# Optimization experiments

Hardware: AMD Instinct MI355X
Metric: run time of the kernel (lower is better)

## Reference

```python
import jax, jax.numpy as jnp
import numpy as np

POLY_DEGREE = 2
LEVELS = 3


def setup_inputs() -> dict:
    key = jax.random.key(0)
    B, T, C = 32, 4096, 128
    x = jax.random.normal(key, (B, T, C), dtype=jnp.float32)
    return {"x": x}


def reference(x):
    B, T, C = x.shape
    t = jnp.linspace(0.0, 1.0, T, dtype=x.dtype)[:, None]          # [T,1]
    Tmat = jnp.concatenate([t ** i for i in range(POLY_DEGREE + 1)], axis=1)  # [T,d+1]
    # Least-squares solution is identical across batch & channel since the
    # design matrix is shared: sol = pinv(Tmat) @ x  (closed-form, one solve).
    P = jnp.linalg.pinv(Tmat)                                       # [d+1,T]
    coef = jnp.einsum('dt,btc->bdc', P, x)                          # [B,d+1,C]
    low = jnp.einsum('td,bdc->btc', Tmat, coef)                     # [B,T,C] trend
    res = x - low                                                   # residual
    highs = [res] + [jnp.zeros_like(res) for _ in range(LEVELS - 1)]
    return (low, highs)
```

## Files before the change

kernel.cpp:

```cpp
#include <hip/hip_runtime.h>
#include <hip/hip_cooperative_groups.h>

namespace cg = cooperative_groups;

typedef float f4 __attribute__((ext_vector_type(4)));

#define TT 4096
#define CC 128
#define BB 32
#define C4 (CC / 4)
#define NB 1024
#define ROWS_B 128
#define RECS 32

__global__ __launch_bounds__(256, 4) void k_fused(const f4* __restrict__ x4,
                                                  f4* __restrict__ partial,
                                                  f4* __restrict__ out,
                                                  float scale, float c20,
                                                  float invS0, float invS2,
                                                  float invD) {
    const size_t N4 = (size_t)BB * TT * C4;
    const int blk = blockIdx.x;
    const int b = blk >> 5;
    const int tile = blk & 31;
    const int tid = threadIdx.x;
    const int r = tid >> 5;
    const int q = tid & 31;

    __shared__ f4 red[3][8][32];
    __shared__ f4 ca[3][32];

    const size_t base = (size_t)b * TT * C4;
    const int t0 = tile * ROWS_B;
    const f4 z = (f4)0.0f;

    f4 m0 = (f4)0.0f, m1 = (f4)0.0f, m2 = (f4)0.0f;
#pragma unroll
    for (int k = 0; k < ROWS_B / 8; ++k) {
        const int t = t0 + r + (k << 3);
        const float u = fmaf((float)t, scale, -0.5f);
        const size_t idx = base + (size_t)t * C4 + q;
        const f4 v = x4[idx];
        m0 += v;
        m1 += u * v;
        m2 += (u * u) * v;
        __builtin_nontemporal_store(z, &out[2 * N4 + idx]);
        __builtin_nontemporal_store(z, &out[3 * N4 + idx]);
    }
    red[0][r][q] = m0;
    red[1][r][q] = m1;
    red[2][r][q] = m2;
    __syncthreads();
    if (tid < 32) {
#pragma unroll
        for (int j = 0; j < 3; ++j) {
            f4 acc = red[j][0][tid];
#pragma unroll
            for (int rr = 1; rr < 8; ++rr) acc += red[j][rr][tid];
            partial[(size_t)blk * (3 * C4) + j * C4 + tid] = acc;
        }
    }

    cg::this_grid().sync();

    const f4* pb = partial + (size_t)b * (RECS * 3 * C4);
#pragma unroll
    for (int j = 0; j < 3; ++j) {
        f4 acc = (f4)0.0f;
#pragma unroll
        for (int k = 0; k < 4; ++k)
            acc += pb[(size_t)(4 * r + k) * (3 * C4) + j * C4 + q];
        red[j][r][q] = acc;
    }
    __syncthreads();
    if (tid < 32) {
        f4 s0 = (f4)0.0f, s1 = (f4)0.0f, s2 = (f4)0.0f;
#pragma unroll
        for (int rr = 0; rr < 8; ++rr) {
            s0 += red[0][rr][tid];
            s1 += red[1][rr][tid];
            s2 += red[2][rr][tid];
        }
        ca[0][tid] = s0 * invS0;
        ca[1][tid] = s1 * invS2;
        ca[2][tid] = (s2 - c20 * s0) * invD;
    }
    __syncthreads();

    const f4 a0 = ca[0][q];
    const f4 a1 = ca[1][q];
    const f4 a2 = ca[2][q];

#pragma unroll
    for (int k = 0; k < ROWS_B / 8; ++k) {
        const int t = t0 + r + (k << 3);
        const float u = fmaf((float)t, scale, -0.5f);
        const float w = fmaf(u, u, -c20);
        const size_t idx = base + (size_t)t * C4 + q;
        const f4 xv = x4[idx];
        const f4 lo = a0 + u * a1 + w * a2;
        const f4 re = xv - lo;
        __builtin_nontemporal_store(lo, &out[idx]);
        __builtin_nontemporal_store(re, &out[N4 + idx]);
    }
}

#define NGM 16
#define SLAB (TT / NGM)
#define NTILE 64

__global__ __launch_bounds__(256) void k_moments_zero(const f4* __restrict__ x4,
                                                      f4* __restrict__ partial,
                                                      f4* __restrict__ out,
                                                      float scale) {
    const size_t N4 = (size_t)BB * TT * C4;
    const int blk = blockIdx.x;
    const int tid = threadIdx.x;
    const int r = tid >> 5;
    const int q = tid & 31;

    if (blk < BB * NGM) {
        const int b = blk >> 4;
        const int s = blk & 15;
        const f4* xb = x4 + (size_t)b * TT * C4;
        const int t0 = s * SLAB;
        f4 m0 = (f4)0.0f, m1 = (f4)0.0f, m2 = (f4)0.0f;
#pragma unroll 8
        for (int k = 0; k < SLAB / 8; ++k) {
            const int t = t0 + r + (k << 3);
            const float u = fmaf((float)t, scale, -0.5f);
            const f4 v = xb[(size_t)t * C4 + q];
            m0 += v;
            m1 += u * v;
            m2 += (u * u) * v;
        }
        __shared__ f4 red[3][8][32];
        red[0][r][q] = m0;
        red[1][r][q] = m1;
        red[2][r][q] = m2;
        __syncthreads();
        if (tid < 32) {
#pragma unroll
            for (int j = 0; j < 3; ++j) {
                f4 acc = red[j][0][tid];
#pragma unroll
                for (int rr = 1; rr < 8; ++rr) acc += red[j][rr][tid];
                partial[(size_t)blk * (3 * C4) + j * C4 + tid] = acc;
            }
        }
    } else {
        const int zid = blk - BB * NGM;
        const int b = zid >> 6;
        const int tile = zid & 63;
        const size_t base = (size_t)b * TT * C4 + (size_t)(tile * 64) * C4;
        const f4 z = (f4)0.0f;
#pragma unroll
        for (int k = 0; k < 8; ++k) {
            const size_t idx = base + (size_t)(r + (k << 3)) * C4 + q;
            __builtin_nontemporal_store(z, &out[2 * N4 + idx]);
            __builtin_nontemporal_store(z, &out[3 * N4 + idx]);
        }
    }
}

__global__ __launch_bounds__(256) void k_emit(const f4* __restrict__ x4,
                                              const f4* __restrict__ partial,
                                              f4* __restrict__ out,
                                              float scale, float c20,
                                              float invS0, float invS2,
                                              float invD) {
    const size_t N4 = (size_t)BB * TT * C4;
    const int blk = blockIdx.x;
    const int b = blk >> 6;
    const int tile = blk & 63;
    const int tid = threadIdx.x;
    const int r = tid >> 5;
    const int q = tid & 31;

    __shared__ f4 red[3][8][32];
    __shared__ f4 ca[3][32];

    const f4* pb = partial + (size_t)b * (NGM * 3 * C4);
#pragma unroll
    for (int j = 0; j < 3; ++j) {
        const f4 e0 = pb[(size_t)(2 * r + 0) * (3 * C4) + j * C4 + q];
        const f4 e1 = pb[(size_t)(2 * r + 1) * (3 * C4) + j * C4 + q];
        red[j][r][q] = e0 + e1;
    }
    __syncthreads();
    if (tid < 32) {
        f4 s0 = (f4)0.0f, s1 = (f4)0.0f, s2 = (f4)0.0f;
#pragma unroll
        for (int rr = 0; rr < 8; ++rr) {
            s0 += red[0][rr][tid];
            s1 += red[1][rr][tid];
            s2 += red[2][rr][tid];
        }
        ca[0][tid] = s0 * invS0;
        ca[1][tid] = s1 * invS2;
        ca[2][tid] = (s2 - c20 * s0) * invD;
    }
    __syncthreads();

    const f4 a0 = ca[0][q];
    const f4 a1 = ca[1][q];
    const f4 a2 = ca[2][q];

    const size_t base = (size_t)b * TT * C4;
    const int t0 = tile * 64;
#pragma unroll
    for (int k = 0; k < 8; ++k) {
        const int t = t0 + r + (k << 3);
        const float u = fmaf((float)t, scale, -0.5f);
        const float w = fmaf(u, u, -c20);
        const size_t idx = base + (size_t)t * C4 + q;
        const f4 xv = x4[idx];
        const f4 lo = a0 + u * a1 + w * a2;
        const f4 re = xv - lo;
        __builtin_nontemporal_store(lo, &out[idx]);
        __builtin_nontemporal_store(re, &out[N4 + idx]);
    }
}

extern "C" void kernel_launch(void* const* d_in, const int* in_sizes, int n_in,
                              void* d_out, int out_size, void* d_ws, size_t ws_size,
                              hipStream_t stream) {
    const float* x = (const float*)d_in[0];
    float* out = (float*)d_out;
    const size_t N = (size_t)BB * TT * CC;

    double S0 = (double)TT, S2 = 0.0, S4 = 0.0;
    for (int i = 0; i < TT; ++i) {
        double u = (double)i / (double)(TT - 1) - 0.5;
        double u2 = u * u;
        S2 += u2;
        S4 += u2 * u2;
    }
    const double c20d = S2 / S0;
    const double Dd = S4 - S2 * S2 / S0;
    float scale = (float)(1.0 / (double)(TT - 1));
    float invS0 = (float)(1.0 / S0);
    float invS2 = (float)(1.0 / S2);
    float invD  = (float)(1.0 / Dd);
    float c20   = (float)c20d;

    const size_t coop_need = (size_t)NB * 3 * C4 * sizeof(f4);

    if (ws_size >= coop_need) {
        int dev = 0, coop = 0, cus = 0, occ = 0;
        if (hipGetDevice(&dev) == hipSuccess &&
            hipDeviceGetAttribute(&coop, hipDeviceAttributeCooperativeLaunch,
                                  dev) == hipSuccess &&
            coop &&
            hipDeviceGetAttribute(&cus, hipDeviceAttributeMultiprocessorCount,
                                  dev) == hipSuccess &&
            hipOccupancyMaxActiveBlocksPerMultiprocessor(
                &occ, (const void*)k_fused, 256, 0) == hipSuccess &&
            occ * cus >= NB) {
            const f4* x4 = (const f4*)x;
            f4* partial = (f4*)d_ws;
            f4* out4 = (f4*)out;
            void* args[] = {(void*)&x4, (void*)&partial, (void*)&out4,
                            (void*)&scale, (void*)&c20,
                            (void*)&invS0, (void*)&invS2, (void*)&invD};
            hipError_t err = hipLaunchCooperativeKernel(
                (const void*)k_fused, dim3(NB), dim3(256), args, 0, stream);
            if (err == hipSuccess) return;
        }
    }

    const size_t fb_need = (size_t)BB * NGM * 3 * C4 * sizeof(f4);
    if (ws_size >= fb_need) {
        f4* partial = (f4*)d_ws;
        k_moments_zero<<<BB * NGM + BB * NTILE, 256, 0, stream>>>(
            (const f4*)x, partial, (f4*)out, scale);
        k_emit<<<BB * NTILE, 256, 0, stream>>>(
            (const f4*)x, partial, (f4*)out, scale, c20, invS0, invS2, invD);
    } else {
        f4* partial = (f4*)(out + 2 * N);
        k_moments_zero<<<BB * NGM, 256, 0, stream>>>(
            (const f4*)x, partial, (f4*)out, scale);
        k_emit<<<BB * NTILE, 256, 0, stream>>>(
            (const f4*)x, partial, (f4*)out, scale, c20, invS0, invS2, invD);
        hipMemsetAsync(out + 2 * N, 0, 2 * N * sizeof(float), stream);
    }
}
```

Measured before the change: 61.73 us.

## Replace grid-wide sync with per-batch atomic counter barrier and remap blocks

Replaces the cooperative-groups grid sync with a per-batch arrival counter, so each batch's 32 tiles only wait for each other instead of for the whole grid. The block-to-(batch,tile) mapping is also permuted so a batch's tiles are spread across block indices, which may place them on different XCDs or CUs. A memset of the counters is added before the launch, and the spin-wait uses acquire loads with sleep and a bounded spin count. This risks extra launch overhead from the memset and relies on co-residency still being guaranteed by the cooperative launch.

After: 61.71 us. No clear change (-0.0%).

```diff
diff --git a/kernel.cpp b/kernel.cpp
--- a/kernel.cpp
+++ b/kernel.cpp
@@ -1,7 +1,5 @@
 #include <hip/hip_runtime.h>
 #include <hip/hip_cooperative_groups.h>
-
-namespace cg = cooperative_groups;
 
 typedef float f4 __attribute__((ext_vector_type(4)));
 
@@ -15,14 +13,15 @@
 
 __global__ __launch_bounds__(256, 4) void k_fused(const f4* __restrict__ x4,
                                                   f4* __restrict__ partial,
+                                                  int* __restrict__ ctr,
                                                   f4* __restrict__ out,
                                                   float scale, float c20,
                                                   float invS0, float invS2,
                                                   float invD) {
     const size_t N4 = (size_t)BB * TT * C4;
     const int blk = blockIdx.x;
-    const int b = blk >> 5;
-    const int tile = blk & 31;
+    const int b = ((blk & 7) << 2) + (blk >> 8);
+    const int tile = (blk >> 3) & 31;
     const int tid = threadIdx.x;
     const int r = tid >> 5;
     const int q = tid & 31;
@@ -57,11 +56,24 @@
             f4 acc = red[j][0][tid];
 #pragma unroll
             for (int rr = 1; rr < 8; ++rr) acc += red[j][rr][tid];
-            partial[(size_t)blk * (3 * C4) + j * C4 + tid] = acc;
-        }
-    }
-
-    cg::this_grid().sync();
+            partial[(size_t)(b * RECS + tile) * (3 * C4) + j * C4 + tid] = acc;
+        }
+        __threadfence();
+    }
+    __syncthreads();
+
+    if (tid == 0) {
+        atomicAdd(&ctr[b], 1);
+        int spins = 0;
+        while (__hip_atomic_load(&ctr[b], __ATOMIC_ACQUIRE,
+                                 __HIP_MEMORY_SCOPE_AGENT) < RECS &&
+               spins < (1 << 27)) {
+            __builtin_amdgcn_s_sleep(2);
+            ++spins;
+        }
+    }
+    __syncthreads();
+    __threadfence();
 
     const f4* pb = partial + (size_t)b * (RECS * 3 * C4);
 #pragma unroll
@@ -244,7 +256,9 @@
     float invD  = (float)(1.0 / Dd);
     float c20   = (float)c20d;
 
-    const size_t coop_need = (size_t)NB * 3 * C4 * sizeof(f4);
+    const size_t partial_bytes = (size_t)NB * 3 * C4 * sizeof(f4);
+    const size_t ctr_bytes     = BB * sizeof(int);
+    const size_t coop_need     = partial_bytes + ctr_bytes;
 
     if (ws_size >= coop_need) {
         int dev = 0, coop = 0, cus = 0, occ = 0;
@@ -259,9 +273,11 @@
             occ * cus >= NB) {
             const f4* x4 = (const f4*)x;
             f4* partial = (f4*)d_ws;
+            int* ctr = (int*)((char*)d_ws + partial_bytes);
             f4* out4 = (f4*)out;
-            void* args[] = {(void*)&x4, (void*)&partial, (void*)&out4,
-                            (void*)&scale, (void*)&c20,
+            hipMemsetAsync(ctr, 0, ctr_bytes, stream);
+            void* args[] = {(void*)&x4, (void*)&partial, (void*)&ctr,
+                            (void*)&out4, (void*)&scale, (void*)&c20,
                             (void*)&invS0, (void*)&invS2, (void*)&invD};
             hipError_t err = hipLaunchCooperativeKernel(
                 (const void*)k_fused, dim3(NB), dim3(256), args, 0, stream);
```
